# Optimization experiments

Hardware: AMD Instinct MI355X
Metric: run time of the kernel (lower is better)

The kernel has to match this reference:

```python
import jax, jax.numpy as jnp
import numpy as np

B, N, E = 8, 2048, 1024


def setup_inputs() -> dict:
    key = jax.random.key(0)
    x = jax.random.normal(key, (B, N, E), dtype=jnp.float32)
    pos = jnp.ones((N - 1,), dtype=jnp.float32)
    zero = jnp.ones((1,), dtype=jnp.float32)
    neg = jnp.ones((N - 1,), dtype=jnp.float32)
    return {"x": x, "pos": pos, "zero": zero, "neg": neg}


def reference(x, pos, zero, neg):
    # x: [b, n, e]; Toeplitz matvec via circular FFT convolution of length 2n.
    b, n, e = x.shape
    # circulant kernel: [zero, pos[:n-1], zero, neg[-(n-1):]] -> length 2n
    a = jnp.concatenate([zero, pos[: n - 1], zero, neg[-(n - 1):]])
    # torch: fft(x, 2n, dim=1, norm='ortho')
    y = jnp.fft.fft(x, n=2 * n, axis=1, norm="ortho")  # [b, 2n, e] complex
    # torch: fft(a) with default ('backward') norm, i.e. unnormalized forward
    v = jnp.fft.fft(a)[None, :, None]                   # [1, 2n, 1]
    u = v * y
    out = jnp.fft.ifft(u, n=2 * n, axis=1, norm="ortho")[:, :n, :].real
    return out.astype(x.dtype)
```

## Files before the change

kernel.cpp:

```cpp
#include <hip/hip_runtime.h>
#include <stdint.h>


#define B_ 8
#define N_ 2048
#define NF 4096
#define E_ 1024

__device__ __forceinline__ int P(int n) {
    return n ^ ((n >> 4) & 15) ^ ((n >> 8) & 15) ^ (((n >> 9) & 1) << 4);
}
#define PERM(r) ((((r) & 3) << 2) | ((r) >> 2))

__device__ __forceinline__ uint32_t cpack(float re, float im) {
    uint32_t r;
    asm("v_cvt_pk_bf16_f32 %0, %1, %2" : "=v"(r) : "v"(re), "v"(im));
    return r;
}
__device__ __forceinline__ void cunpack(uint32_t u, float& re, float& im) {
    union { uint32_t u; float f; } a, b;
    a.u = u << 16; b.u = u & 0xffff0000u;
    re = a.f; im = b.f;
}
__device__ __forceinline__ void cmul(float& ar, float& ai, float br, float bi) {
    float t = ar * br - ai * bi; ai = ar * bi + ai * br; ar = t;
}
__device__ __forceinline__ void cmulc(float& ar, float& ai, float br, float bi) {
    float t = ar * br + ai * bi; ai = ai * br - ar * bi; ar = t;
}

__device__ __forceinline__ void dft4(float& x0r, float& x0i, float& x1r, float& x1i,
                                     float& x2r, float& x2i, float& x3r, float& x3i,
                                     float sg) {
    float t0r = x0r + x2r, t0i = x0i + x2i;
    float t1r = x0r - x2r, t1i = x0i - x2i;
    float t2r = x1r + x3r, t2i = x1i + x3i;
    float t3r = x1r - x3r, t3i = x1i - x3i;
    x0r = t0r + t2r; x0i = t0i + t2i;
    x2r = t0r - t2r; x2i = t0i - t2i;
    x1r = t1r - sg * t3i; x1i = t1i + sg * t3r;
    x3r = t1r + sg * t3i; x3i = t1i - sg * t3r;
}

template<int SG>
__device__ __forceinline__ void dft16_layer1(float* xr, float* xi) {
    const float sg = (float)SG;
#pragma unroll
    for (int n0 = 0; n0 < 4; ++n0)
        dft4(xr[n0], xi[n0], xr[n0 + 4], xi[n0 + 4],
             xr[n0 + 8], xi[n0 + 8], xr[n0 + 12], xi[n0 + 12], sg);
}
template<int SG>
__device__ __forceinline__ void dft16_layer1_pad(float* xr, float* xi) {
    const float sg = (float)SG;
#pragma unroll
    for (int n0 = 0; n0 < 4; ++n0) {
        float ar = xr[n0], ai = xi[n0], br = xr[n0 + 4], bi = xi[n0 + 4];
        xr[n0]      = ar + br;       xi[n0]      = ai + bi;
        xr[n0 + 4]  = ar - sg * bi;  xi[n0 + 4]  = ai + sg * br;
        xr[n0 + 8]  = ar - br;       xi[n0 + 8]  = ai - bi;
        xr[n0 + 12] = ar + sg * bi;  xi[n0 + 12] = ai - sg * br;
    }
}
template<int SG>
__device__ __forceinline__ void dft16_twiddle(float* xr, float* xi) {
    const float sg = (float)SG;
    const float C1 = 0.923879532511286756f;
    const float S1 = 0.382683432365089772f;
    const float H  = 0.707106781186547524f;
    cmul(xr[5],  xi[5],  C1,  sg * S1);
    cmul(xr[9],  xi[9],  H,   sg * H);
    cmul(xr[13], xi[13], S1,  sg * C1);
    cmul(xr[6],  xi[6],  H,   sg * H);
    cmul(xr[10], xi[10], 0.f, sg);
    cmul(xr[14], xi[14], -H,  sg * H);
    cmul(xr[7],  xi[7],  S1,  sg * C1);
    cmul(xr[11], xi[11], -H,  sg * H);
    cmul(xr[15], xi[15], -C1, -sg * S1);
}
template<int SG>
__device__ __forceinline__ void dft16_layer2(float* xr, float* xi) {
    const float sg = (float)SG;
#pragma unroll
    for (int k1 = 0; k1 < 4; ++k1)
        dft4(xr[4 * k1], xi[4 * k1], xr[4 * k1 + 1], xi[4 * k1 + 1],
             xr[4 * k1 + 2], xi[4 * k1 + 2], xr[4 * k1 + 3], xi[4 * k1 + 3], sg);
}
template<int SG>
__device__ __forceinline__ void dft16(float* xr, float* xi) {
    dft16_layer1<SG>(xr, xi);
    dft16_twiddle<SG>(xr, xi);
    dft16_layer2<SG>(xr, xi);
}

template<int L>
__device__ __forceinline__ void fwd_stage_sincos(float2* buf, int t) {
    constexpr int Lq = L / 16;
    int g = t / Lq;
    int j = t - g * Lq;
    int base = g * L + j;
    const float TPI = -6.28318530717958647692f;
    float xr[16], xi[16];
#pragma unroll
    for (int r = 0; r < 16; ++r) {
        float2 v = buf[P(base + r * Lq)];
        xr[r] = v.x; xi[r] = v.y;
    }
    dft16<-1>(xr, xi);
    { float2 v; v.x = xr[0]; v.y = xi[0]; buf[P(base)] = v; }
#pragma unroll
    for (int r = 1; r < 16; ++r) {
        float s, c;
        __sincosf(TPI * (float)(j * r) * (1.f / (float)L), &s, &c);
        float yr = xr[PERM(r)], yi = xi[PERM(r)];
        cmul(yr, yi, c, s);
        float2 v; v.x = yr; v.y = yi;
        buf[P(base + r * Lq)] = v;
    }
}

__global__ __launch_bounds__(256) void prep(const float* __restrict__ x,
                                            const float* __restrict__ pos,
                                            const float* __restrict__ zero,
                                            const float* __restrict__ neg,
                                            uint32_t* __restrict__ xP,
                                            float2* __restrict__ tw4096,
                                            float2* __restrict__ tw256,
                                            float2* __restrict__ V2) {
    __shared__ __align__(16) char smraw[32768];
    const float TPI = -6.28318530717958647692f;
    int blk = blockIdx.x, t = threadIdx.x;
    if (blk < 16) {
        float s, c;
        __sincosf(TPI * (float)(blk * t) * (1.f / 4096.f), &s, &c);
        float2 v; v.x = c; v.y = s;
        tw4096[blk * 256 + t] = v;
    } else if (blk == 16) {
        int r = t >> 4, j = t & 15;
        float s, c;
        __sincosf(TPI * (float)(r * j) * (1.f / 256.f), &s, &c);
        float2 v; v.x = c; v.y = s;
        tw256[t] = v;
    } else if (blk == 17) {
        float2* buf = (float2*)smraw;
#pragma unroll
        for (int it = 0; it < 16; ++it) {
            int n = t + 256 * it;
            float v;
            if (n == 0) v = zero[0];
            else if (n < N_) v = pos[n - 1];
            else if (n == N_) v = zero[0];
            else v = neg[n - (N_ + 1)];
            float2 cc; cc.x = v; cc.y = 0.f;
            buf[P(n)] = cc;
        }
        __syncthreads();
        fwd_stage_sincos<4096>(buf, t); __syncthreads();
        fwd_stage_sincos<256>(buf, t);  __syncthreads();
        fwd_stage_sincos<16>(buf, t);   __syncthreads();
        const float s = 1.f / (float)NF;
#pragma unroll
        for (int it = 0; it < 16; ++it) {
            int n = t + 256 * it;
            float2 c = buf[P(n)];
            c.x *= s; c.y *= s;
            V2[n] = c;
        }
    } else {
        float (*tile)[66] = (float (*)[66])smraw;
        int tid = blk - 18;
        int e0 = (tid & 15) * 64;
        int j0 = ((tid >> 4) & 31) * 64;
        int b  = tid >> 9;
        int e4 = t & 15, jr = t >> 4;
#pragma unroll
        for (int it = 0; it < 4; ++it) {
            int j = jr + it * 16;
            const float4 v = *(const float4*)(x + ((size_t)(b * N_ + j0 + j) * E_) + e0 + e4 * 4);
            tile[e4 * 4 + 0][j] = v.x;
            tile[e4 * 4 + 1][j] = v.y;
            tile[e4 * 4 + 2][j] = v.z;
            tile[e4 * 4 + 3][j] = v.w;
        }
        __syncthreads();
        int jj = t & 63, ur = t >> 6;
#pragma unroll
        for (int it = 0; it < 8; ++it) {
            int u = ur + it * 4;
            uint32_t w = cpack(tile[2 * u][jj], tile[2 * u + 1][jj]);
            xP[((size_t)(b * 512 + (e0 >> 1) + u)) * N_ + j0 + jj] = w;
        }
    }
}

__global__ __launch_bounds__(256) void fft_conv(const uint32_t* __restrict__ xP,
                                                const float2* __restrict__ tw4096,
                                                const float2* __restrict__ tw256,
                                                const float2* __restrict__ V2,
                                                float* __restrict__ out) {
    __shared__ uint32_t buf0[NF];
    __shared__ uint32_t buf1[NF];
    int t = threadIdx.x;
    int bid = blockIdx.x;
    int xcd = bid & 7;
    int q = bid >> 3;
    int b = q >> 5;
    int quad = xcd * 32 + (q & 31);
    const uint32_t* g0 = xP + ((size_t)(b * 512 + quad * 2)) * N_;
    const uint32_t* g1 = g0 + N_;

    float x0r[16], x0i[16], x1r[16], x1i[16];

#pragma unroll
    for (int r = 0; r < 8; ++r) {
        int n = t + 256 * r;
        cunpack(g0[n], x0r[r], x0i[r]);
        cunpack(g1[n], x1r[r], x1i[r]);
    }
#pragma unroll
    for (int r = 8; r < 16; ++r) { x0r[r] = 0.f; x0i[r] = 0.f; x1r[r] = 0.f; x1i[r] = 0.f; }
    dft16_layer1_pad<-1>(x0r, x0i); dft16_layer1_pad<-1>(x1r, x1i);
    dft16_twiddle<-1>(x0r, x0i);    dft16_twiddle<-1>(x1r, x1i);
    dft16_layer2<-1>(x0r, x0i);     dft16_layer2<-1>(x1r, x1i);
    buf0[P(t)] = cpack(x0r[0], x0i[0]);
    buf1[P(t)] = cpack(x1r[0], x1i[0]);
#pragma unroll
    for (int r = 1; r < 16; ++r) {
        float2 w = tw4096[r * 256 + t];
        int a = P(t + 256 * r);
        float y0r = x0r[PERM(r)], y0i = x0i[PERM(r)];
        cmul(y0r, y0i, w.x, w.y);
        buf0[a] = cpack(y0r, y0i);
        float y1r = x1r[PERM(r)], y1i = x1i[PERM(r)];
        cmul(y1r, y1i, w.x, w.y);
        buf1[a] = cpack(y1r, y1i);
    }
    __syncthreads();

    int g = t >> 4, j = t & 15;
    int base = g * 256 + j;
#pragma unroll
    for (int r = 0; r < 16; ++r) {
        int a = P(base + 16 * r);
        cunpack(buf0[a], x0r[r], x0i[r]);
        cunpack(buf1[a], x1r[r], x1i[r]);
    }
    dft16<-1>(x0r, x0i); dft16<-1>(x1r, x1i);
    buf0[P(base)] = cpack(x0r[0], x0i[0]);
    buf1[P(base)] = cpack(x1r[0], x1i[0]);
#pragma unroll
    for (int r = 1; r < 16; ++r) {
        float2 w = tw256[r * 16 + j];
        int a = P(base + 16 * r);
        float y0r = x0r[PERM(r)], y0i = x0i[PERM(r)];
        cmul(y0r, y0i, w.x, w.y);
        buf0[a] = cpack(y0r, y0i);
        float y1r = x1r[PERM(r)], y1i = x1i[PERM(r)];
        cmul(y1r, y1i, w.x, w.y);
        buf1[a] = cpack(y1r, y1i);
    }
    __syncthreads();

    {
        int mb = 16 * t;
#pragma unroll
        for (int r = 0; r < 16; ++r) {
            int a = P(mb + r);
            cunpack(buf0[a], x0r[r], x0i[r]);
            cunpack(buf1[a], x1r[r], x1i[r]);
        }
        dft16<-1>(x0r, x0i); dft16<-1>(x1r, x1i);
#pragma unroll
        for (int r = 0; r < 16; ++r) {
            int p = PERM(r);
            if (p < r) continue;
            if (p == r) {
                float2 vv = V2[mb + r];
                float ar = x0r[r], ai = x0i[r];
                x0r[r] = ar * vv.x - ai * vv.y; x0i[r] = ar * vv.y + ai * vv.x;
                ar = x1r[r]; ai = x1i[r];
                x1r[r] = ar * vv.x - ai * vv.y; x1i[r] = ar * vv.y + ai * vv.x;
            } else {
                float2 va = V2[mb + r], vb = V2[mb + p];
                float ar = x0r[r], ai = x0i[r], br = x0r[p], bi = x0i[p];
                x0r[r] = br * va.x - bi * va.y; x0i[r] = br * va.y + bi * va.x;
                x0r[p] = ar * vb.x - ai * vb.y; x0i[p] = ar * vb.y + ai * vb.x;
                ar = x1r[r]; ai = x1i[r]; br = x1r[p]; bi = x1i[p];
                x1r[r] = br * va.x - bi * va.y; x1i[r] = br * va.y + bi * va.x;
                x1r[p] = ar * vb.x - ai * vb.y; x1i[p] = ar * vb.y + ai * vb.x;
            }
        }
        dft16<1>(x0r, x0i); dft16<1>(x1r, x1i);
#pragma unroll
        for (int r = 0; r < 16; ++r) {
            int a = P(mb + r);
            buf0[a] = cpack(x0r[PERM(r)], x0i[PERM(r)]);
            buf1[a] = cpack(x1r[PERM(r)], x1i[PERM(r)]);
        }
    }
    __syncthreads();

#pragma unroll
    for (int r = 0; r < 16; ++r) {
        int a = P(base + 16 * r);
        cunpack(buf0[a], x0r[r], x0i[r]);
        cunpack(buf1[a], x1r[r], x1i[r]);
    }
#pragma unroll
    for (int r = 1; r < 16; ++r) {
        float2 w = tw256[r * 16 + j];
        cmulc(x0r[r], x0i[r], w.x, w.y);
        cmulc(x1r[r], x1i[r], w.x, w.y);
    }
    dft16<1>(x0r, x0i); dft16<1>(x1r, x1i);
#pragma unroll
    for (int r = 0; r < 16; ++r) {
        int a = P(base + 16 * r);
        buf0[a] = cpack(x0r[PERM(r)], x0i[PERM(r)]);
        buf1[a] = cpack(x1r[PERM(r)], x1i[PERM(r)]);
    }
    __syncthreads();

#pragma unroll
    for (int r = 0; r < 16; ++r) {
        int a = P(t + 256 * r);
        cunpack(buf0[a], x0r[r], x0i[r]);
        cunpack(buf1[a], x1r[r], x1i[r]);
    }
#pragma unroll
    for (int r = 1; r < 16; ++r) {
        float2 w = tw4096[r * 256 + t];
        cmulc(x0r[r], x0i[r], w.x, w.y);
        cmulc(x1r[r], x1i[r], w.x, w.y);
    }
    dft16_layer1<1>(x0r, x0i); dft16_layer1<1>(x1r, x1i);
    dft16_twiddle<1>(x0r, x0i); dft16_twiddle<1>(x1r, x1i);
    float* ob = out + ((size_t)b * N_) * E_ + quad * 4;
#pragma unroll
    for (int k1 = 0; k1 < 4; ++k1) {
        float a0r = x0r[4 * k1],     a0i = x0i[4 * k1];
        float a1r = x0r[4 * k1 + 1], a1i = x0i[4 * k1 + 1];
        float a2r = x0r[4 * k1 + 2], a2i = x0i[4 * k1 + 2];
        float a3r = x0r[4 * k1 + 3], a3i = x0i[4 * k1 + 3];
        float t0r = a0r + a2r, t0i = a0i + a2i;
        float t1r = a0r - a2r, t1i = a0i - a2i;
        float t2r = a1r + a3r, t2i = a1i + a3i;
        float t3r = a1r - a3r, t3i = a1i - a3i;
        float s0v0r = t0r + t2r, s0v0i = t0i + t2i;
        float s0v1r = t1r - t3i, s0v1i = t1i + t3r;
        a0r = x1r[4 * k1];     a0i = x1i[4 * k1];
        a1r = x1r[4 * k1 + 1]; a1i = x1i[4 * k1 + 1];
        a2r = x1r[4 * k1 + 2]; a2i = x1i[4 * k1 + 2];
        a3r = x1r[4 * k1 + 3]; a3i = x1i[4 * k1 + 3];
        t0r = a0r + a2r; t0i = a0i + a2i;
        t1r = a0r - a2r; t1i = a0i - a2i;
        t2r = a1r + a3r; t2i = a1i + a3i;
        t3r = a1r - a3r; t3i = a1i - a3i;
        float s1v0r = t0r + t2r, s1v0i = t0i + t2i;
        float s1v1r = t1r - t3i, s1v1i = t1i + t3r;
        float4 w0; w0.x = s0v0r; w0.y = s0v0i; w0.z = s1v0r; w0.w = s1v0i;
        float4 w1; w1.x = s0v1r; w1.y = s0v1i; w1.z = s1v1r; w1.w = s1v1i;
        *(float4*)(ob + (size_t)(t + 256 * k1) * E_)       = w0;
        *(float4*)(ob + (size_t)(t + 256 * (k1 + 4)) * E_) = w1;
    }
}

__global__ __launch_bounds__(256) void naive_toep(const float* __restrict__ x,
                                                  const float* __restrict__ pos,
                                                  const float* __restrict__ zero,
                                                  const float* __restrict__ neg,
                                                  float* __restrict__ out) {
    int bid = blockIdx.x;
    int e   = (bid & 3) * 256 + threadIdx.x;
    int k   = (bid >> 2) & (N_ - 1);
    int b   = bid >> 13;
    float zv = zero[0];
    float acc = 0.f;
    const float* xb = x + (size_t)b * N_ * E_ + e;
    for (int jj = 0; jj < N_; ++jj) {
        float c = (jj < k) ? pos[k - jj - 1] : (jj == k) ? zv : neg[N_ - 1 - jj + k];
        acc += c * xb[(size_t)jj * E_];
    }
    out[((size_t)(b * N_ + k)) * E_ + e] = acc;
}

extern "C" void kernel_launch(void* const* d_in, const int* in_sizes, int n_in,
                              void* d_out, int out_size, void* d_ws, size_t ws_size,
                              hipStream_t stream) {
    const float* x    = (const float*)d_in[0];
    const float* pos  = (const float*)d_in[1];
    const float* zero = (const float*)d_in[2];
    const float* neg  = (const float*)d_in[3];
    float* out = (float*)d_out;

    const size_t needX = (size_t)B_ * 512 * N_ * sizeof(uint32_t);
    const size_t need  = needX + (2 * (size_t)NF + 256) * sizeof(float2);
    if (ws_size >= need) {
        uint32_t* xP   = (uint32_t*)d_ws;
        float2* tw4096 = (float2*)((char*)d_ws + needX);
        float2* tw256  = tw4096 + NF;
        float2* V2     = tw256 + 256;
        prep<<<18 + 4096, 256, 0, stream>>>(x, pos, zero, neg, xP, tw4096, tw256, V2);
        fft_conv<<<2048, 256, 0, stream>>>(xP, tw4096, tw256, V2, out);
    } else {
        naive_toep<<<65536, 256, 0, stream>>>(x, pos, zero, neg, out);
    }
}
```

Before: 170.5 us.

## Process one packed column pair per block to raise occupancy

```diff
diff --git a/kernel.cpp b/kernel.cpp
--- a/kernel.cpp
+++ b/kernel.cpp
@@ -193,37 +193,31 @@
     }
 }
 
-__global__ __launch_bounds__(256) void fft_conv(const uint32_t* __restrict__ xP,
-                                                const float2* __restrict__ tw4096,
-                                                const float2* __restrict__ tw256,
-                                                const float2* __restrict__ V2,
-                                                float* __restrict__ out) {
+__global__ __launch_bounds__(256, 5) void fft_conv(const uint32_t* __restrict__ xP,
+                                                   const float2* __restrict__ tw4096,
+                                                   const float2* __restrict__ tw256,
+                                                   const float2* __restrict__ V2,
+                                                   float* __restrict__ out) {
     __shared__ uint32_t buf0[NF];
-    __shared__ uint32_t buf1[NF];
     int t = threadIdx.x;
     int bid = blockIdx.x;
-    int xcd = bid & 7;
-    int q = bid >> 3;
-    int b = q >> 5;
-    int quad = xcd * 32 + (q & 31);
-    const uint32_t* g0 = xP + ((size_t)(b * 512 + quad * 2)) * N_;
-    const uint32_t* g1 = g0 + N_;
-
-    float x0r[16], x0i[16], x1r[16], x1i[16];
+    int b = bid & 7;
+    int u = bid >> 3;
+    const uint32_t* g0 = xP + ((size_t)(b * 512 + u)) * N_;
+
+    float x0r[16], x0i[16];
 
 #pragma unroll
     for (int r = 0; r < 8; ++r) {
         int n = t + 256 * r;
         cunpack(g0[n], x0r[r], x0i[r]);
-        cunpack(g1[n], x1r[r], x1i[r]);
-    }
-#pragma unroll
-    for (int r = 8; r < 16; ++r) { x0r[r] = 0.f; x0i[r] = 0.f; x1r[r] = 0.f; x1i[r] = 0.f; }
-    dft16_layer1_pad<-1>(x0r, x0i); dft16_layer1_pad<-1>(x1r, x1i);
-    dft16_twiddle<-1>(x0r, x0i);    dft16_twiddle<-1>(x1r, x1i);
-    dft16_layer2<-1>(x0r, x0i);     dft16_layer2<-1>(x1r, x1i);
+    }
+#pragma unroll
+    for (int r = 8; r < 16; ++r) { x0r[r] = 0.f; x0i[r] = 0.f; }
+    dft16_layer1_pad<-1>(x0r, x0i);
+    dft16_twiddle<-1>(x0r, x0i);
+    dft16_layer2<-1>(x0r, x0i);
     buf0[P(t)] = cpack(x0r[0], x0i[0]);
-    buf1[P(t)] = cpack(x1r[0], x1i[0]);
 #pragma unroll
     for (int r = 1; r < 16; ++r) {
         float2 w = tw4096[r * 256 + t];
@@ -231,9 +225,6 @@
         float y0r = x0r[PERM(r)], y0i = x0i[PERM(r)];
         cmul(y0r, y0i, w.x, w.y);
         buf0[a] = cpack(y0r, y0i);
-        float y1r = x1r[PERM(r)], y1i = x1i[PERM(r)];
-        cmul(y1r, y1i, w.x, w.y);
-        buf1[a] = cpack(y1r, y1i);
     }
     __syncthreads();
 
@@ -243,11 +234,9 @@
     for (int r = 0; r < 16; ++r) {
         int a = P(base + 16 * r);
         cunpack(buf0[a], x0r[r], x0i[r]);
-        cunpack(buf1[a], x1r[r], x1i[r]);
-    }
-    dft16<-1>(x0r, x0i); dft16<-1>(x1r, x1i);
+    }
+    dft16<-1>(x0r, x0i);
     buf0[P(base)] = cpack(x0r[0], x0i[0]);
-    buf1[P(base)] = cpack(x1r[0], x1i[0]);
 #pragma unroll
     for (int r = 1; r < 16; ++r) {
         float2 w = tw256[r * 16 + j];
@@ -255,9 +244,6 @@
         float y0r = x0r[PERM(r)], y0i = x0i[PERM(r)];
         cmul(y0r, y0i, w.x, w.y);
         buf0[a] = cpack(y0r, y0i);
-        float y1r = x1r[PERM(r)], y1i = x1i[PERM(r)];
-        cmul(y1r, y1i, w.x, w.y);
-        buf1[a] = cpack(y1r, y1i);
     }
     __syncthreads();
 
@@ -267,9 +253,8 @@
         for (int r = 0; r < 16; ++r) {
             int a = P(mb + r);
             cunpack(buf0[a], x0r[r], x0i[r]);
-            cunpack(buf1[a], x1r[r], x1i[r]);
-        }
-        dft16<-1>(x0r, x0i); dft16<-1>(x1r, x1i);
+        }
+        dft16<-1>(x0r, x0i);
 #pragma unroll
         for (int r = 0; r < 16; ++r) {
             int p = PERM(r);
@@ -278,24 +263,18 @@
                 float2 vv = V2[mb + r];
                 float ar = x0r[r], ai = x0i[r];
                 x0r[r] = ar * vv.x - ai * vv.y; x0i[r] = ar * vv.y + ai * vv.x;
-                ar = x1r[r]; ai = x1i[r];
-                x1r[r] = ar * vv.x - ai * vv.y; x1i[r] = ar * vv.y + ai * vv.x;
             } else {
                 float2 va = V2[mb + r], vb = V2[mb + p];
                 float ar = x0r[r], ai = x0i[r], br = x0r[p], bi = x0i[p];
                 x0r[r] = br * va.x - bi * va.y; x0i[r] = br * va.y + bi * va.x;
                 x0r[p] = ar * vb.x - ai * vb.y; x0i[p] = ar * vb.y + ai * vb.x;
-                ar = x1r[r]; ai = x1i[r]; br = x1r[p]; bi = x1i[p];
-                x1r[r] = br * va.x - bi * va.y; x1i[r] = br * va.y + bi * va.x;
-                x1r[p] = ar * vb.x - ai * vb.y; x1i[p] = ar * vb.y + ai * vb.x;
             }
         }
-        dft16<1>(x0r, x0i); dft16<1>(x1r, x1i);
+        dft16<1>(x0r, x0i);
 #pragma unroll
         for (int r = 0; r < 16; ++r) {
             int a = P(mb + r);
             buf0[a] = cpack(x0r[PERM(r)], x0i[PERM(r)]);
-            buf1[a] = cpack(x1r[PERM(r)], x1i[PERM(r)]);
         }
     }
     __syncthreads();
@@ -304,20 +283,17 @@
     for (int r = 0; r < 16; ++r) {
         int a = P(base + 16 * r);
         cunpack(buf0[a], x0r[r], x0i[r]);
-        cunpack(buf1[a], x1r[r], x1i[r]);
     }
 #pragma unroll
     for (int r = 1; r < 16; ++r) {
         float2 w = tw256[r * 16 + j];
         cmulc(x0r[r], x0i[r], w.x, w.y);
-        cmulc(x1r[r], x1i[r], w.x, w.y);
-    }
-    dft16<1>(x0r, x0i); dft16<1>(x1r, x1i);
+    }
+    dft16<1>(x0r, x0i);
 #pragma unroll
     for (int r = 0; r < 16; ++r) {
         int a = P(base + 16 * r);
         buf0[a] = cpack(x0r[PERM(r)], x0i[PERM(r)]);
-        buf1[a] = cpack(x1r[PERM(r)], x1i[PERM(r)]);
     }
     __syncthreads();
 
@@ -325,17 +301,15 @@
     for (int r = 0; r < 16; ++r) {
         int a = P(t + 256 * r);
         cunpack(buf0[a], x0r[r], x0i[r]);
-        cunpack(buf1[a], x1r[r], x1i[r]);
     }
 #pragma unroll
     for (int r = 1; r < 16; ++r) {
         float2 w = tw4096[r * 256 + t];
         cmulc(x0r[r], x0i[r], w.x, w.y);
-        cmulc(x1r[r], x1i[r], w.x, w.y);
-    }
-    dft16_layer1<1>(x0r, x0i); dft16_layer1<1>(x1r, x1i);
-    dft16_twiddle<1>(x0r, x0i); dft16_twiddle<1>(x1r, x1i);
-    float* ob = out + ((size_t)b * N_) * E_ + quad * 4;
+    }
+    dft16_layer1<1>(x0r, x0i);
+    dft16_twiddle<1>(x0r, x0i);
+    float* ob = out + ((size_t)b * N_) * E_ + u * 2;
 #pragma unroll
     for (int k1 = 0; k1 < 4; ++k1) {
         float a0r = x0r[4 * k1],     a0i = x0i[4 * k1];
@@ -346,22 +320,10 @@
         float t1r = a0r - a2r, t1i = a0i - a2i;
         float t2r = a1r + a3r, t2i = a1i + a3i;
         float t3r = a1r - a3r, t3i = a1i - a3i;
-        float s0v0r = t0r + t2r, s0v0i = t0i + t2i;
-        float s0v1r = t1r - t3i, s0v1i = t1i + t3r;
-        a0r = x1r[4 * k1];     a0i = x1i[4 * k1];
-        a1r = x1r[4 * k1 + 1]; a1i = x1i[4 * k1 + 1];
-        a2r = x1r[4 * k1 + 2]; a2i = x1i[4 * k1 + 2];
-        a3r = x1r[4 * k1 + 3]; a3i = x1i[4 * k1 + 3];
-        t0r = a0r + a2r; t0i = a0i + a2i;
-        t1r = a0r - a2r; t1i = a0i - a2i;
-        t2r = a1r + a3r; t2i = a1i + a3i;
-        t3r = a1r - a3r; t3i = a1i - a3i;
-        float s1v0r = t0r + t2r, s1v0i = t0i + t2i;
-        float s1v1r = t1r - t3i, s1v1i = t1i + t3r;
-        float4 w0; w0.x = s0v0r; w0.y = s0v0i; w0.z = s1v0r; w0.w = s1v0i;
-        float4 w1; w1.x = s0v1r; w1.y = s0v1i; w1.z = s1v1r; w1.w = s1v1i;
-        *(float4*)(ob + (size_t)(t + 256 * k1) * E_)       = w0;
-        *(float4*)(ob + (size_t)(t + 256 * (k1 + 4)) * E_) = w1;
+        float2 w0; w0.x = t0r + t2r; w0.y = t0i + t2i;
+        float2 w1; w1.x = t1r - t3i; w1.y = t1i + t3r;
+        *(float2*)(ob + (size_t)(t + 256 * k1) * E_)       = w0;
+        *(float2*)(ob + (size_t)(t + 256 * (k1 + 4)) * E_) = w1;
     }
 }
 
@@ -401,7 +363,7 @@
         float2* tw256  = tw4096 + NF;
         float2* V2     = tw256 + 256;
         prep<<<18 + 4096, 256, 0, stream>>>(x, pos, zero, neg, xP, tw4096, tw256, V2);
-        fft_conv<<<2048, 256, 0, stream>>>(xP, tw4096, tw256, V2, out);
+        fft_conv<<<4096, 256, 0, stream>>>(xP, tw4096, tw256, V2, out);
     } else {
         naive_toep<<<65536, 256, 0, stream>>>(x, pos, zero, neg, out);
     }
```

New measurement: 238.4 us. 1.4x slower.
